# Kernel optimization log

Measured on AMD Instinct MI355X. Metric: run time of the kernel, lower is better.

The kernel has to match this reference:

```python
import jax, jax.numpy as jnp
import numpy as np

B, S, D, H = 4, 2048, 768, 12
HD = D // H           # 64, also BigBird block size
BS, NB = 64, S // 64  # block size, num blocks
DFF = 4 * D
NEG = jnp.float32(-1e9)


def _bigbird_block_mask():
    # window(3) + global(first/last block rows+cols) + 3 random blocks per row
    rng = np.random.default_rng(0)
    m = np.zeros((NB, NB), dtype=bool)
    idx = np.arange(NB)
    for off in (-1, 0, 1):
        m[idx, np.clip(idx + off, 0, NB - 1)] = True
    m[0, :] = True; m[-1, :] = True; m[:, 0] = True; m[:, -1] = True
    rand_cols = rng.integers(0, NB, size=(NB, 3))
    m[idx[:, None], rand_cols] = True
    return m


def setup_inputs() -> dict:
    key = jax.random.key(0)
    ks = jax.random.split(key, 12)
    sc = 0.02
    inp = {
        "q": jax.random.normal(ks[0], (B, S, D), jnp.float32),
        "encoder_out": jax.random.normal(ks[1], (B, S, D), jnp.float32),
        "bb_mask": jnp.asarray(_bigbird_block_mask()),
        "Wq_s": jax.random.normal(ks[2], (D, D), jnp.float32) * sc,
        "Wk_s": jax.random.normal(ks[3], (D, D), jnp.float32) * sc,
        "Wv_s": jax.random.normal(ks[4], (D, D), jnp.float32) * sc,
        "Wo_s": jax.random.normal(ks[5], (D, D), jnp.float32) * sc,
        "Wq_c": jax.random.normal(ks[6], (D, D), jnp.float32) * sc,
        "Wk_c": jax.random.normal(ks[7], (D, D), jnp.float32) * sc,
        "Wv_c": jax.random.normal(ks[8], (D, D), jnp.float32) * sc,
        "Wo_c": jax.random.normal(ks[9], (D, D), jnp.float32) * sc,
        "ln_g": jnp.ones((D,), jnp.float32),
        "ln_b": jnp.zeros((D,), jnp.float32),
        "W1": jax.random.normal(ks[10], (D, DFF), jnp.float32) * sc,
        "b1": jnp.zeros((DFF,), jnp.float32),
        "W2": jax.random.normal(ks[11], (DFF, D), jnp.float32) * sc,
        "b2": jnp.zeros((D,), jnp.float32),
    }
    return inp


def _ln(x, g, b):
    mu = jnp.mean(x, -1, keepdims=True)
    var = jnp.mean(jnp.square(x - mu), -1, keepdims=True)
    return (x - mu) * jax.lax.rsqrt(var + 1e-5) * g + b


def _mha(xq, xkv, Wq, Wk, Wv, Wo, mask):
    # mask: [Sq, Sk] bool, True = attend
    b, sq, _ = xq.shape
    sk = xkv.shape[1]
    q = (xq @ Wq).reshape(b, sq, H, HD).transpose(0, 2, 1, 3)
    k = (xkv @ Wk).reshape(b, sk, H, HD).transpose(0, 2, 1, 3)
    v = (xkv @ Wv).reshape(b, sk, H, HD).transpose(0, 2, 1, 3)
    scores = jnp.einsum('bhqd,bhkd->bhqk', q, k) / jnp.sqrt(jnp.float32(HD))
    scores = jnp.where(mask[None, None], scores, NEG)
    attn = jax.nn.softmax(scores, axis=-1)
    o = jnp.einsum('bhqk,bhkd->bhqd', attn, v).transpose(0, 2, 1, 3).reshape(b, sq, D)
    return o @ Wo


def reference(q, encoder_out, bb_mask,
              Wq_s, Wk_s, Wv_s, Wo_s,
              Wq_c, Wk_c, Wv_c, Wo_c,
              ln_g, ln_b, W1, b1, W2, b2):
    # expand block mask to element level [S, S]
    el = jnp.repeat(jnp.repeat(bb_mask, BS, axis=0), BS, axis=1)
    causal = jnp.tril(jnp.ones((S, S), bool))
    m_self = el & causal
    x = q + _mha(_ln(q, ln_g, ln_b), _ln(q, ln_g, ln_b), Wq_s, Wk_s, Wv_s, Wo_s, m_self)
    x = x + _mha(_ln(x, ln_g, ln_b), encoder_out, Wq_c, Wk_c, Wv_c, Wo_c, el)
    h = _ln(x, ln_g, ln_b)
    x = x + (jax.nn.relu(h @ W1 + b1) @ W2 + b2)
    return x
```

## Files before the change

kernel.cpp:

```cpp
#include <hip/hip_runtime.h>
#include <hip/hip_bf16.h>

#define S_LEN 2048
#define DIM   768
#define NHEAD 12
#define HDIM  64
#define NBLK  32
#define BTOK  8192
#define DFF_  3072

typedef __attribute__((ext_vector_type(8))) short bf16x8;
typedef __attribute__((ext_vector_type(4))) float f32x4;

__device__ __forceinline__ void glds16(const void* g, void* l) {
  __builtin_amdgcn_global_load_lds(
      (const __attribute__((address_space(1))) void*)g,
      (__attribute__((address_space(3))) void*)l, 16, 0, 0);
}

__device__ __forceinline__ unsigned short bfbits(float f) {
  __hip_bfloat16 t = __float2bfloat16(f);
  return *(unsigned short*)&t;
}

__global__ void mask_norm_k(const unsigned char* __restrict__ p,
                            unsigned char* __restrict__ out) {
  int i = blockIdx.x * 256 + threadIdx.x;
  if (i < NBLK * NBLK) {
    bool byteLayout = (p[1] != 0);
    out[i] = byteLayout ? (unsigned char)(p[i] != 0)
                        : (unsigned char)(((const int*)p)[i] != 0);
  }
}

__device__ __forceinline__ float blockReduceSum256(float v) {
  v += __shfl_down(v, 32); v += __shfl_down(v, 16); v += __shfl_down(v, 8);
  v += __shfl_down(v, 4);  v += __shfl_down(v, 2);  v += __shfl_down(v, 1);
  __shared__ float sm[4];
  int w = threadIdx.x >> 6;
  __syncthreads();
  if ((threadIdx.x & 63) == 0) sm[w] = v;
  __syncthreads();
  return sm[0] + sm[1] + sm[2] + sm[3];
}

__global__ __launch_bounds__(256) void ln_k(const float* __restrict__ x,
                                            const float* __restrict__ g,
                                            const float* __restrict__ b,
                                            __hip_bfloat16* __restrict__ y) {
  size_t row = blockIdx.x;
  const float* xr = x + row * DIM;
  int t = threadIdx.x;
  float v0 = xr[t], v1 = xr[t + 256], v2 = xr[t + 512];
  float tot = blockReduceSum256(v0 + v1 + v2);
  float mu = tot * (1.0f / DIM);
  float d0 = v0 - mu, d1 = v1 - mu, d2 = v2 - mu;
  float var = blockReduceSum256(d0 * d0 + d1 * d1 + d2 * d2) * (1.0f / DIM);
  float rstd = rsqrtf(var + 1e-5f);
  __hip_bfloat16* yr = y + row * DIM;
  yr[t]       = __float2bfloat16(d0 * rstd * g[t]       + b[t]);
  yr[t + 256] = __float2bfloat16(d1 * rstd * g[t + 256] + b[t + 256]);
  yr[t + 512] = __float2bfloat16(d2 * rstd * g[t + 512] + b[t + 512]);
}

__global__ __launch_bounds__(256) void castbf_k(const float* __restrict__ x,
                                                __hip_bfloat16* __restrict__ y,
                                                int n) {
  int i = (blockIdx.x * 256 + threadIdx.x) * 8;
  if (i < n) {
    float4 v0 = *(const float4*)(x + i);
    float4 v1 = *(const float4*)(x + i + 4);
    union { bf16x8 v; unsigned short u[8]; } pk;
    pk.u[0] = bfbits(v0.x); pk.u[1] = bfbits(v0.y);
    pk.u[2] = bfbits(v0.z); pk.u[3] = bfbits(v0.w);
    pk.u[4] = bfbits(v1.x); pk.u[5] = bfbits(v1.y);
    pk.u[6] = bfbits(v1.z); pk.u[7] = bfbits(v1.w);
    *(bf16x8*)((unsigned short*)y + i) = pk.v;
  }
}

__global__ __launch_bounds__(256) void tcast_k(const float* __restrict__ W,
                                               __hip_bfloat16* __restrict__ Wt,
                                               int R, int C) {
  __shared__ float T[64][65];
  int r0 = blockIdx.y * 64, c0 = blockIdx.x * 64;
  int t = threadIdx.x;
  int r = t >> 2, cg = (t & 3) * 16;
  #pragma unroll
  for (int ii = 0; ii < 16; ii += 4) {
    float4 v = *(const float4*)(W + (size_t)(r0 + r) * C + c0 + cg + ii);
    T[r][cg + ii + 0] = v.x; T[r][cg + ii + 1] = v.y;
    T[r][cg + ii + 2] = v.z; T[r][cg + ii + 3] = v.w;
  }
  __syncthreads();
  int oc = t >> 2, og = (t & 3) * 16;
  union { bf16x8 v; unsigned short u[8]; } p0, p1;
  #pragma unroll
  for (int ii = 0; ii < 8; ++ii) p0.u[ii] = bfbits(T[og + ii][oc]);
  #pragma unroll
  for (int ii = 0; ii < 8; ++ii) p1.u[ii] = bfbits(T[og + 8 + ii][oc]);
  unsigned short* dst = (unsigned short*)Wt + (size_t)(c0 + oc) * R + r0 + og;
  *(bf16x8*)dst = p0.v;
  *(bf16x8*)(dst + 8) = p1.v;
}

template<bool BF16OUT, bool HASBIAS, bool HASRES, bool RELU, bool TRANSV>
__global__ __launch_bounds__(256) void mgemm_k(
    const __hip_bfloat16* __restrict__ A,
    const __hip_bfloat16* __restrict__ Bt,
    const float* __restrict__ bias,
    const float* __restrict__ resid,
    void* __restrict__ Cout,
    int M, int N, int K) {
  __shared__ char Asl[128 * 128];
  __shared__ char Bsl[128 * 128];
  int tid = threadIdx.x, w = tid >> 6, lane = tid & 63;
  int g = lane >> 4, cc = lane & 15;
  int wr = w >> 1, wc = w & 1;
  int m0 = blockIdx.y * 128, n0 = blockIdx.x * 128;

  f32x4 acc[4][4];
  #pragma unroll
  for (int i = 0; i < 4; ++i)
    #pragma unroll
    for (int j = 0; j < 4; ++j) acc[i][j] = (f32x4){0.f, 0.f, 0.f, 0.f};

  for (int k0 = 0; k0 < K; k0 += 64) {
    __syncthreads();
    #pragma unroll
    for (int ii = 0; ii < 4; ++ii) {
      int chunk = ii * 256 + w * 64 + lane;
      int row = chunk >> 3, hh = chunk & 7;
      int koff = k0 + ((hh ^ (row & 7)) << 3);
      glds16(A  + (size_t)(m0 + row) * K + koff, Asl + (ii * 256 + w * 64) * 16);
      glds16(Bt + (size_t)(n0 + row) * K + koff, Bsl + (ii * 256 + w * 64) * 16);
    }
    __syncthreads();
    bf16x8 a[4][2], b[4][2];
    #pragma unroll
    for (int i = 0; i < 4; ++i)
      #pragma unroll
      for (int s = 0; s < 2; ++s) {
        int row = wr * 64 + i * 16 + cc;
        a[i][s] = *(const bf16x8*)(Asl + row * 128 + (((s * 4 + g) ^ (cc & 7)) << 4));
      }
    #pragma unroll
    for (int j = 0; j < 4; ++j)
      #pragma unroll
      for (int s = 0; s < 2; ++s) {
        int row = wc * 64 + j * 16 + cc;
        b[j][s] = *(const bf16x8*)(Bsl + row * 128 + (((s * 4 + g) ^ (cc & 7)) << 4));
      }
    #pragma unroll
    for (int i = 0; i < 4; ++i)
      #pragma unroll
      for (int j = 0; j < 4; ++j)
        #pragma unroll
        for (int s = 0; s < 2; ++s)
          acc[i][j] = __builtin_amdgcn_mfma_f32_16x16x32_bf16(a[i][s], b[j][s], acc[i][j], 0, 0, 0);
  }
  #pragma unroll
  for (int i = 0; i < 4; ++i)
    #pragma unroll
    for (int j = 0; j < 4; ++j)
      #pragma unroll
      for (int e = 0; e < 4; ++e) {
        int r   = m0 + wr * 64 + i * 16 + g * 4 + e;
        int col = n0 + wc * 64 + j * 16 + cc;
        float v = acc[i][j][e];
        if (HASBIAS) v += bias[col];
        if (HASRES)  v += resid[(size_t)r * N + col];
        if (RELU)    v = fmaxf(v, 0.f);
        if (TRANSV) {
          int bb = r >> 11, s = r & 2047;
          ((__hip_bfloat16*)Cout)[(size_t)bb * DIM * S_LEN + (size_t)col * S_LEN + s] = __float2bfloat16(v);
        } else if (BF16OUT) {
          ((__hip_bfloat16*)Cout)[(size_t)r * N + col] = __float2bfloat16(v);
        } else {
          ((float*)Cout)[(size_t)r * N + col] = v;
        }
      }
}

template<bool CAUSAL>
__global__ __launch_bounds__(256) void mattn_k(
    const __hip_bfloat16* __restrict__ Qg,
    const __hip_bfloat16* __restrict__ Kg,
    const __hip_bfloat16* __restrict__ Vtg,
    __hip_bfloat16* __restrict__ O,
    const unsigned char* __restrict__ mask) {
  __shared__ char Qs[8192], Ks[8192], Vs[8192], Ps[8192];
  int qb = blockIdx.x, h = blockIdx.y, b = blockIdx.z;
  int t = threadIdx.x, w = t >> 6, lane = t & 63;
  int g = lane >> 4, cc = lane & 15;

  #pragma unroll
  for (int ii = 0; ii < 2; ++ii) {
    int chunk = ii * 256 + w * 64 + lane;
    int qr = chunk >> 3, hh = chunk & 7;
    glds16(Qg + (size_t)(b * S_LEN + qb * 64 + qr) * DIM + h * HDIM + ((hh ^ (qr & 7)) << 3),
           Qs + (ii * 256 + w * 64) * 16);
  }
  __syncthreads();
  bf16x8 aq[2];
  #pragma unroll
  for (int s = 0; s < 2; ++s) {
    int row = w * 16 + cc;
    aq[s] = *(const bf16x8*)(Qs + row * 128 + (((s * 4 + g) ^ (cc & 7)) << 4));
  }

  float m_[4], l_[4];
  f32x4 accO[4];
  #pragma unroll
  for (int e = 0; e < 4; ++e) { m_[e] = -3.0e38f; l_[e] = 0.f; }
  #pragma unroll
  for (int j = 0; j < 4; ++j) accO[j] = (f32x4){0.f, 0.f, 0.f, 0.f};

  int kbEnd = CAUSAL ? (qb + 1) : NBLK;
  for (int kb = 0; kb < kbEnd; ++kb) {
    if (!mask[qb * NBLK + kb]) continue;
    __syncthreads();
    #pragma unroll
    for (int ii = 0; ii < 2; ++ii) {
      int chunk = ii * 256 + w * 64 + lane;
      int rr = chunk >> 3, hh = chunk & 7;
      glds16(Kg + (size_t)(b * S_LEN + kb * 64 + rr) * DIM + h * HDIM + ((hh ^ (rr & 7)) << 3),
             Ks + (ii * 256 + w * 64) * 16);
      glds16(Vtg + (size_t)b * DIM * S_LEN + (size_t)(h * HDIM + rr) * S_LEN + kb * 64 + ((hh ^ (rr & 7)) << 3),
             Vs + (ii * 256 + w * 64) * 16);
    }
    __syncthreads();

    f32x4 S[4];
    #pragma unroll
    for (int j = 0; j < 4; ++j) S[j] = (f32x4){0.f, 0.f, 0.f, 0.f};
    #pragma unroll
    for (int j = 0; j < 4; ++j)
      #pragma unroll
      for (int s = 0; s < 2; ++s) {
        int kv = j * 16 + cc;
        bf16x8 bk = *(const bf16x8*)(Ks + kv * 128 + (((s * 4 + g) ^ (cc & 7)) << 4));
        S[j] = __builtin_amdgcn_mfma_f32_16x16x32_bf16(aq[s], bk, S[j], 0, 0, 0);
      }

    float p_[4][4];
    #pragma unroll
    for (int e = 0; e < 4; ++e) {
      float mm = -3.0e38f;
      #pragma unroll
      for (int j = 0; j < 4; ++j) {
        float sv = S[j][e] * 0.125f;
        if (CAUSAL && kb == qb) {
          int ql = w * 16 + g * 4 + e, kl = j * 16 + cc;
          if (kl > ql) sv = -1e9f;
        }
        p_[j][e] = sv;
        mm = fmaxf(mm, sv);
      }
      mm = fmaxf(mm, __shfl_xor(mm, 1));
      mm = fmaxf(mm, __shfl_xor(mm, 2));
      mm = fmaxf(mm, __shfl_xor(mm, 4));
      mm = fmaxf(mm, __shfl_xor(mm, 8));
      float newm = fmaxf(m_[e], mm);
      float corr = expf(m_[e] - newm);
      float rs = 0.f;
      #pragma unroll
      for (int j = 0; j < 4; ++j) {
        float p = expf(p_[j][e] - newm);
        p_[j][e] = p;
        rs += p;
      }
      rs += __shfl_xor(rs, 1); rs += __shfl_xor(rs, 2);
      rs += __shfl_xor(rs, 4); rs += __shfl_xor(rs, 8);
      l_[e] = l_[e] * corr + rs;
      m_[e] = newm;
      #pragma unroll
      for (int j = 0; j < 4; ++j) accO[j][e] *= corr;
      int ql = g * 4 + e;
      #pragma unroll
      for (int j = 0; j < 4; ++j) {
        int kv = j * 16 + cc;
        int byt = w * 2048 + ql * 128 + ((((kv >> 3) ^ (ql & 7))) << 4) + ((kv & 7) << 1);
        *(unsigned short*)(Ps + byt) = bfbits(p_[j][e]);
      }
    }
    #pragma unroll
    for (int s = 0; s < 2; ++s) {
      bf16x8 ap = *(const bf16x8*)(Ps + w * 2048 + cc * 128 + (((s * 4 + g) ^ (cc & 7)) << 4));
      #pragma unroll
      for (int j = 0; j < 4; ++j) {
        int d = j * 16 + cc;
        bf16x8 bv = *(const bf16x8*)(Vs + d * 128 + (((s * 4 + g) ^ (cc & 7)) << 4));
        accO[j] = __builtin_amdgcn_mfma_f32_16x16x32_bf16(ap, bv, accO[j], 0, 0, 0);
      }
    }
  }
  #pragma unroll
  for (int e = 0; e < 4; ++e) {
    float inv = 1.0f / fmaxf(l_[e], 1e-30f);
    int tok = b * S_LEN + qb * 64 + w * 16 + g * 4 + e;
    #pragma unroll
    for (int j = 0; j < 4; ++j)
      O[(size_t)tok * DIM + h * HDIM + j * 16 + cc] = __float2bfloat16(accO[j][e] * inv);
  }
}

extern "C" void kernel_launch(void* const* d_in, const int* in_sizes, int n_in,
                              void* d_out, int out_size, void* d_ws, size_t ws_size,
                              hipStream_t stream) {
  const float* q    = (const float*)d_in[0];
  const float* enc  = (const float*)d_in[1];
  const unsigned char* bbm = (const unsigned char*)d_in[2];
  const float* Wsrc[8] = {(const float*)d_in[3], (const float*)d_in[4],
                          (const float*)d_in[5], (const float*)d_in[6],
                          (const float*)d_in[7], (const float*)d_in[8],
                          (const float*)d_in[9], (const float*)d_in[10]};
  const float* ln_g = (const float*)d_in[11];
  const float* ln_b = (const float*)d_in[12];
  const float* W1   = (const float*)d_in[13];
  const float* b1   = (const float*)d_in[14];
  const float* W2   = (const float*)d_in[15];
  const float* b2   = (const float*)d_in[16];

  char* ws = (char*)d_ws;
  unsigned char* maskn = (unsigned char*)ws;
  const size_t WT1 = (size_t)DIM * DIM * 2;
  __hip_bfloat16* Wt[8];
  for (int i = 0; i < 8; ++i) Wt[i] = (__hip_bfloat16*)(ws + 4096 + i * WT1);
  __hip_bfloat16* W1t  = (__hip_bfloat16*)(ws + 9441280);
  __hip_bfloat16* W2t  = (__hip_bfloat16*)(ws + 14159872);
  __hip_bfloat16* Ebf  = (__hip_bfloat16*)(ws + 18878464);
  float*          X    = (float*)         (ws + 31461376);
  __hip_bfloat16* Abf  = (__hip_bfloat16*)(ws + 56627200);
  __hip_bfloat16* Bq   = (__hip_bfloat16*)(ws + 69210112);
  __hip_bfloat16* Bk   = (__hip_bfloat16*)(ws + 81793024);
  __hip_bfloat16* Vt   = (__hip_bfloat16*)(ws + 94375936);
  __hip_bfloat16* Cc   = (__hip_bfloat16*)(ws + 106958848);
  __hip_bfloat16* F    = Bq;

  dim3 blk(256);
  dim3 gsq(12, 12), gw1(48, 12), gw2(12, 48);
  dim3 g768(6, 64), gff(24, 64);
  dim3 ga(NBLK, NHEAD, 4);

  mask_norm_k<<<4, blk, 0, stream>>>(bbm, maskn);
  for (int i = 0; i < 8; ++i)
    tcast_k<<<gsq, blk, 0, stream>>>(Wsrc[i], Wt[i], DIM, DIM);
  tcast_k<<<gw1, blk, 0, stream>>>(W1, W1t, DIM, DFF_);
  tcast_k<<<gw2, blk, 0, stream>>>(W2, W2t, DFF_, DIM);
  castbf_k<<<3072, blk, 0, stream>>>(enc, Ebf, BTOK * DIM);

  ln_k<<<BTOK, blk, 0, stream>>>(q, ln_g, ln_b, Abf);
  mgemm_k<true,false,false,false,false><<<g768, blk, 0, stream>>>(Abf, Wt[0], nullptr, nullptr, Bq, BTOK, DIM, DIM);
  mgemm_k<true,false,false,false,false><<<g768, blk, 0, stream>>>(Abf, Wt[1], nullptr, nullptr, Bk, BTOK, DIM, DIM);
  mgemm_k<true,false,false,false,true ><<<g768, blk, 0, stream>>>(Abf, Wt[2], nullptr, nullptr, Vt, BTOK, DIM, DIM);
  mattn_k<true><<<ga, blk, 0, stream>>>(Bq, Bk, Vt, Cc, maskn);
  mgemm_k<false,false,true,false,false><<<g768, blk, 0, stream>>>(Cc, Wt[3], nullptr, q, X, BTOK, DIM, DIM);

  ln_k<<<BTOK, blk, 0, stream>>>(X, ln_g, ln_b, Abf);
  mgemm_k<true,false,false,false,false><<<g768, blk, 0, stream>>>(Abf, Wt[4], nullptr, nullptr, Bq, BTOK, DIM, DIM);
  mgemm_k<true,false,false,false,false><<<g768, blk, 0, stream>>>(Ebf, Wt[5], nullptr, nullptr, Bk, BTOK, DIM, DIM);
  mgemm_k<true,false,false,false,true ><<<g768, blk, 0, stream>>>(Ebf, Wt[6], nullptr, nullptr, Vt, BTOK, DIM, DIM);
  mattn_k<false><<<ga, blk, 0, stream>>>(Bq, Bk, Vt, Cc, maskn);
  mgemm_k<false,false,true,false,false><<<g768, blk, 0, stream>>>(Cc, Wt[7], nullptr, X, X, BTOK, DIM, DIM);

  ln_k<<<BTOK, blk, 0, stream>>>(X, ln_g, ln_b, Abf);
  mgemm_k<true,true,false,true,false><<<gff, blk, 0, stream>>>(Abf, W1t, b1, nullptr, F, BTOK, DFF_, DIM);
  mgemm_k<false,true,true,false,false><<<g768, blk, 0, stream>>>(F, W2t, b2, X, d_out, BTOK, DIM, DFF_);

  (void)in_sizes; (void)n_in; (void)out_size; (void)ws_size;
}
```

Baseline: 893.6 us.

## Split attention into single-wave 16-row strips loading K/V directly from global

```diff
diff --git a/kernel.cpp b/kernel.cpp
--- a/kernel.cpp
+++ b/kernel.cpp
@@ -183,31 +183,25 @@
 }
 
 template<bool CAUSAL>
-__global__ __launch_bounds__(256) void mattn_k(
+__global__ __launch_bounds__(64) void mattn_k(
     const __hip_bfloat16* __restrict__ Qg,
     const __hip_bfloat16* __restrict__ Kg,
     const __hip_bfloat16* __restrict__ Vtg,
     __hip_bfloat16* __restrict__ O,
     const unsigned char* __restrict__ mask) {
-  __shared__ char Qs[8192], Ks[8192], Vs[8192], Ps[8192];
-  int qb = blockIdx.x, h = blockIdx.y, b = blockIdx.z;
-  int t = threadIdx.x, w = t >> 6, lane = t & 63;
+  __shared__ char Ps[2048];
+  int strip = blockIdx.x, h = blockIdx.y, b = blockIdx.z;
+  int qb = strip >> 2, wq = strip & 3;
+  int lane = threadIdx.x;
   int g = lane >> 4, cc = lane & 15;
-
-  #pragma unroll
-  for (int ii = 0; ii < 2; ++ii) {
-    int chunk = ii * 256 + w * 64 + lane;
-    int qr = chunk >> 3, hh = chunk & 7;
-    glds16(Qg + (size_t)(b * S_LEN + qb * 64 + qr) * DIM + h * HDIM + ((hh ^ (qr & 7)) << 3),
-           Qs + (ii * 256 + w * 64) * 16);
-  }
-  __syncthreads();
+  const unsigned short* Qp = (const unsigned short*)Qg;
+  const unsigned short* Kp = (const unsigned short*)Kg;
+  const unsigned short* Vp = (const unsigned short*)Vtg;
+
   bf16x8 aq[2];
-  #pragma unroll
-  for (int s = 0; s < 2; ++s) {
-    int row = w * 16 + cc;
-    aq[s] = *(const bf16x8*)(Qs + row * 128 + (((s * 4 + g) ^ (cc & 7)) << 4));
-  }
+  size_t qrow = ((size_t)b * S_LEN + strip * 16 + cc) * DIM + h * HDIM;
+  aq[0] = *(const bf16x8*)(Qp + qrow + g * 8);
+  aq[1] = *(const bf16x8*)(Qp + qrow + (4 + g) * 8);
 
   float m_[4], l_[4];
   f32x4 accO[4];
@@ -219,29 +213,18 @@
   int kbEnd = CAUSAL ? (qb + 1) : NBLK;
   for (int kb = 0; kb < kbEnd; ++kb) {
     if (!mask[qb * NBLK + kb]) continue;
-    __syncthreads();
-    #pragma unroll
-    for (int ii = 0; ii < 2; ++ii) {
-      int chunk = ii * 256 + w * 64 + lane;
-      int rr = chunk >> 3, hh = chunk & 7;
-      glds16(Kg + (size_t)(b * S_LEN + kb * 64 + rr) * DIM + h * HDIM + ((hh ^ (rr & 7)) << 3),
-             Ks + (ii * 256 + w * 64) * 16);
-      glds16(Vtg + (size_t)b * DIM * S_LEN + (size_t)(h * HDIM + rr) * S_LEN + kb * 64 + ((hh ^ (rr & 7)) << 3),
-             Vs + (ii * 256 + w * 64) * 16);
+
+    f32x4 S[4];
+    #pragma unroll
+    for (int j = 0; j < 4; ++j) S[j] = (f32x4){0.f, 0.f, 0.f, 0.f};
+    #pragma unroll
+    for (int j = 0; j < 4; ++j) {
+      size_t krow = ((size_t)b * S_LEN + kb * 64 + j * 16 + cc) * DIM + h * HDIM;
+      bf16x8 bk0 = *(const bf16x8*)(Kp + krow + g * 8);
+      bf16x8 bk1 = *(const bf16x8*)(Kp + krow + (4 + g) * 8);
+      S[j] = __builtin_amdgcn_mfma_f32_16x16x32_bf16(aq[0], bk0, S[j], 0, 0, 0);
+      S[j] = __builtin_amdgcn_mfma_f32_16x16x32_bf16(aq[1], bk1, S[j], 0, 0, 0);
     }
-    __syncthreads();
-
-    f32x4 S[4];
-    #pragma unroll
-    for (int j = 0; j < 4; ++j) S[j] = (f32x4){0.f, 0.f, 0.f, 0.f};
-    #pragma unroll
-    for (int j = 0; j < 4; ++j)
-      #pragma unroll
-      for (int s = 0; s < 2; ++s) {
-        int kv = j * 16 + cc;
-        bf16x8 bk = *(const bf16x8*)(Ks + kv * 128 + (((s * 4 + g) ^ (cc & 7)) << 4));
-        S[j] = __builtin_amdgcn_mfma_f32_16x16x32_bf16(aq[s], bk, S[j], 0, 0, 0);
-      }
 
     float p_[4][4];
     #pragma unroll
@@ -251,7 +234,7 @@
       for (int j = 0; j < 4; ++j) {
         float sv = S[j][e] * 0.125f;
         if (CAUSAL && kb == qb) {
-          int ql = w * 16 + g * 4 + e, kl = j * 16 + cc;
+          int ql = wq * 16 + g * 4 + e, kl = j * 16 + cc;
           if (kl > ql) sv = -1e9f;
         }
         p_[j][e] = sv;
@@ -262,11 +245,11 @@
       mm = fmaxf(mm, __shfl_xor(mm, 4));
       mm = fmaxf(mm, __shfl_xor(mm, 8));
       float newm = fmaxf(m_[e], mm);
-      float corr = expf(m_[e] - newm);
+      float corr = __expf(m_[e] - newm);
       float rs = 0.f;
       #pragma unroll
       for (int j = 0; j < 4; ++j) {
-        float p = expf(p_[j][e] - newm);
+        float p = __expf(p_[j][e] - newm);
         p_[j][e] = p;
         rs += p;
       }
@@ -280,17 +263,18 @@
       #pragma unroll
       for (int j = 0; j < 4; ++j) {
         int kv = j * 16 + cc;
-        int byt = w * 2048 + ql * 128 + ((((kv >> 3) ^ (ql & 7))) << 4) + ((kv & 7) << 1);
+        int byt = ql * 128 + ((((kv >> 3) ^ (ql & 7))) << 4) + ((kv & 7) << 1);
         *(unsigned short*)(Ps + byt) = bfbits(p_[j][e]);
       }
     }
+
     #pragma unroll
     for (int s = 0; s < 2; ++s) {
-      bf16x8 ap = *(const bf16x8*)(Ps + w * 2048 + cc * 128 + (((s * 4 + g) ^ (cc & 7)) << 4));
+      bf16x8 ap = *(const bf16x8*)(Ps + cc * 128 + (((s * 4 + g) ^ (cc & 7)) << 4));
       #pragma unroll
       for (int j = 0; j < 4; ++j) {
-        int d = j * 16 + cc;
-        bf16x8 bv = *(const bf16x8*)(Vs + d * 128 + (((s * 4 + g) ^ (cc & 7)) << 4));
+        size_t vrow = ((size_t)b * DIM + h * HDIM + j * 16 + cc) * S_LEN + kb * 64;
+        bf16x8 bv = *(const bf16x8*)(Vp + vrow + (s * 4 + g) * 8);
         accO[j] = __builtin_amdgcn_mfma_f32_16x16x32_bf16(ap, bv, accO[j], 0, 0, 0);
       }
     }
@@ -298,7 +282,7 @@
   #pragma unroll
   for (int e = 0; e < 4; ++e) {
     float inv = 1.0f / fmaxf(l_[e], 1e-30f);
-    int tok = b * S_LEN + qb * 64 + w * 16 + g * 4 + e;
+    int tok = b * S_LEN + strip * 16 + g * 4 + e;
     #pragma unroll
     for (int j = 0; j < 4; ++j)
       O[(size_t)tok * DIM + h * HDIM + j * 16 + cc] = __float2bfloat16(accO[j][e] * inv);
@@ -341,7 +325,8 @@
   dim3 blk(256);
   dim3 gsq(12, 12), gw1(48, 12), gw2(12, 48);
   dim3 g768(6, 64), gff(24, 64);
-  dim3 ga(NBLK, NHEAD, 4);
+  dim3 ga(128, NHEAD, 4);
+  dim3 wv(64);
 
   mask_norm_k<<<4, blk, 0, stream>>>(bbm, maskn);
   for (int i = 0; i < 8; ++i)
@@ -354,14 +339,14 @@
   mgemm_k<true,false,false,false,false><<<g768, blk, 0, stream>>>(Abf, Wt[0], nullptr, nullptr, Bq, BTOK, DIM, DIM);
   mgemm_k<true,false,false,false,false><<<g768, blk, 0, stream>>>(Abf, Wt[1], nullptr, nullptr, Bk, BTOK, DIM, DIM);
   mgemm_k<true,false,false,false,true ><<<g768, blk, 0, stream>>>(Abf, Wt[2], nullptr, nullptr, Vt, BTOK, DIM, DIM);
-  mattn_k<true><<<ga, blk, 0, stream>>>(Bq, Bk, Vt, Cc, maskn);
+  mattn_k<true><<<ga, wv, 0, stream>>>(Bq, Bk, Vt, Cc, maskn);
   mgemm_k<false,false,true,false,false><<<g768, blk, 0, stream>>>(Cc, Wt[3], nullptr, q, X, BTOK, DIM, DIM);
 
   ln_k<<<BTOK, blk, 0, stream>>>(X, ln_g, ln_b, Abf);
   mgemm_k<true,false,false,false,false><<<g768, blk, 0, stream>>>(Abf, Wt[4], nullptr, nullptr, Bq, BTOK, DIM, DIM);
   mgemm_k<true,false,false,false,false><<<g768, blk, 0, stream>>>(Ebf, Wt[5], nullptr, nullptr, Bk, BTOK, DIM, DIM);
   mgemm_k<true,false,false,false,true ><<<g768, blk, 0, stream>>>(Ebf, Wt[6], nullptr, nullptr, Vt, BTOK, DIM, DIM);
-  mattn_k<false><<<ga, blk, 0, stream>>>(Bq, Bk, Vt, Cc, maskn);
+  mattn_k<false><<<ga, wv, 0, stream>>>(Bq, Bk, Vt, Cc, maskn);
   mgemm_k<false,false,true,false,false><<<g768, blk, 0, stream>>>(Cc, Wt[7], nullptr, X, X, BTOK, DIM, DIM);
 
   ln_k<<<BTOK, blk, 0, stream>>>(X, ln_g, ln_b, Abf);
```

After: 895.8 us. Within noise of the previous version (+0.2%).
